# Kernel optimization log

Measured on AMD Instinct MI355X. Metric: run time of the kernel, lower is better.

Reference implementation:

```python
import jax, jax.numpy as jnp
import numpy as np
import math

D_MODEL = 1024
FEAT = 16            # feature_dim
HEADS = 16
HEAD_DIM = D_MODEL // HEADS          # 64
EXP = 1 + FEAT + FEAT * FEAT         # 273, expanded (Taylor) feature dim
BATCH = 4
SEQ = 2048


def taylor_exp(x):
    """2nd-order Taylor feature map: [1, x/d^{1/4}, (x ox x)/(sqrt(2)*sqrt(d))]."""
    d = x.shape[-1]
    r2 = math.sqrt(2.0)
    rd = math.sqrt(d)
    rrd = math.sqrt(rd)
    x2 = (x[..., :, None] * x[..., None, :]).reshape(*x.shape[:-1], d * d) / r2
    return jnp.concatenate([jnp.ones_like(x[..., :1]), x / rrd, x2 / rd], axis=-1)


def setup_inputs() -> dict:
    key = jax.random.key(0)
    ks = jax.random.split(key, 9)
    s_in = 1.0 / math.sqrt(D_MODEL)
    inp = {
        "x": jax.random.normal(ks[0], (BATCH, SEQ, D_MODEL), dtype=jnp.float32),
        "kv_state": jnp.zeros((BATCH, HEADS, EXP, HEAD_DIM), dtype=jnp.float32),
        "k_state": jnp.zeros((BATCH, HEADS, EXP), dtype=jnp.float32),
        # Linear params stored as [in, out] (y = x @ W + b)
        "Wq": jax.random.normal(ks[1], (D_MODEL, FEAT * HEADS), dtype=jnp.float32) * s_in,
        "bq": jnp.zeros((FEAT * HEADS,), dtype=jnp.float32),
        "Wk": jax.random.normal(ks[2], (D_MODEL, FEAT * HEADS), dtype=jnp.float32) * s_in,
        "bk": jnp.zeros((FEAT * HEADS,), dtype=jnp.float32),
        "Wv": jax.random.normal(ks[3], (D_MODEL, HEAD_DIM * HEADS), dtype=jnp.float32) * s_in,
        "bv": jnp.zeros((HEAD_DIM * HEADS,), dtype=jnp.float32),
        "Wo": jax.random.normal(ks[4], (HEADS * HEAD_DIM, D_MODEL), dtype=jnp.float32) * s_in,
        "bo": jnp.zeros((D_MODEL,), dtype=jnp.float32),
    }
    return inp


def _forward(x, kv_state, k_state, Wq, bq, Wk, bk, Wv, bv, Wo, bo):
    b, l, _ = x.shape
    # projections -> b h l d
    q = (x @ Wq + bq).reshape(b, l, HEADS, FEAT).transpose(0, 2, 1, 3)
    k = (x @ Wk + bk).reshape(b, l, HEADS, FEAT).transpose(0, 2, 1, 3)
    v = (x @ Wv + bv).reshape(b, l, HEADS, HEAD_DIM).transpose(0, 2, 1, 3)
    q = taylor_exp(q)  # b h l EXP
    k = taylor_exp(k)  # b h l EXP

    # scan over time: carry (kv_state [b,h,EXP,hd], k_state [b,h,EXP])
    qs = jnp.moveaxis(q, 2, 0)  # l b h EXP
    ks = jnp.moveaxis(k, 2, 0)  # l b h EXP
    vs = jnp.moveaxis(v, 2, 0)  # l b h hd

    def step(carry, qkv_t):
        kv, kst = carry
        q_t, k_t, v_t = qkv_t
        kv = kv + k_t[..., :, None] * v_t[..., None, :]   # b h EXP hd
        kst = kst + k_t                                    # b h EXP
        num = jnp.einsum('bhd,bhdc->bhc', q_t, kv)
        den = jnp.einsum('bhd,bhd->bh', q_t, kst) + 1e-6
        return (kv, kst), num / den[..., None]

    (kv_f, kst_f), outs = jax.lax.scan(step, (kv_state, k_state), (qs, ks, vs))
    # outs: l b h hd -> b l (h hd)
    y = jnp.moveaxis(outs, 0, 1).reshape(b, l, HEADS * HEAD_DIM)
    y = y @ Wo + bo  # dropout is identity in eval mode
    return y, kv_f, kst_f


def reference(x, kv_state, k_state, Wq, bq, Wk, bk, Wv, bv, Wo, bo):
    return _forward(x, kv_state, k_state, Wq, bq, Wk, bk, Wv, bv, Wo, bo)
```

## Files before the change

### kernel.cpp

```cpp
#include <hip/hip_runtime.h>

typedef unsigned short u16;
typedef __attribute__((ext_vector_type(8))) short bf16x8;
typedef __attribute__((ext_vector_type(4))) float f32x4;

#define BATCH 4
#define SEQ   2048
#define DM    1024
#define HEADS 16
#define FEAT  16
#define HD    64
#define EXPD  273
#define EXPP  288
#define CHK   128
#define NC    16
#define BH    64
#define QKS   512
#define MROWS 8192
#define C2    0.17677669529663687f

__device__ __forceinline__ u16 f2b(float f) {
  union { float f; unsigned u; } v; v.f = f;
  unsigned u = v.u;
  return (u16)((u + 0x7fffu + ((u >> 16) & 1u)) >> 16);
}
__device__ __forceinline__ float b2f(u16 s) {
  union { unsigned u; float f; } v; v.u = ((unsigned)s) << 16; return v.f;
}

typedef const unsigned int __attribute__((address_space(1)))* gas1;
typedef unsigned int __attribute__((address_space(3)))* las3;
__device__ __forceinline__ void gl_lds16(const u16* g, u16* l) {
  __builtin_amdgcn_global_load_lds((gas1)(const void*)g, (las3)(void*)l, 16, 0, 0);
}

__global__ __launch_bounds__(256) void prep(const float* __restrict__ x, u16* __restrict__ xb,
                                            const float* __restrict__ Wq, const float* __restrict__ Wk,
                                            const float* __restrict__ Wv, const float* __restrict__ Wo,
                                            u16* __restrict__ wqkvT, u16* __restrict__ woT,
                                            const float* __restrict__ bq, const float* __restrict__ bk,
                                            const float* __restrict__ bv, float* __restrict__ bias_all) {
  __shared__ float tile[32][33];
  int id = blockIdx.x;
  if (id < 8192) {
    int i = id * 256 + threadIdx.x;
    float4 v = ((const float4*)x)[i];
    u16 r[4] = {f2b(v.x), f2b(v.y), f2b(v.z), f2b(v.w)};
    ((uint2*)xb)[i] = *(uint2*)r;
    return;
  }
  id -= 8192;
  if (id < 2560) {
    const float* src; u16* dst; int N, t;
    if (id < 256)       { src = Wq; dst = wqkvT;            N = 256;  t = id; }
    else if (id < 512)  { src = Wk; dst = wqkvT + 256 * DM; N = 256;  t = id - 256; }
    else if (id < 1536) { src = Wv; dst = wqkvT + 512 * DM; N = 1024; t = id - 512; }
    else                { src = Wo; dst = woT;              N = 1024; t = id - 1536; }
    int nt = N / 32;
    int n0 = (t % nt) * 32, k0 = (t / nt) * 32;
    int tx = threadIdx.x & 31, ty = threadIdx.x >> 5;
    for (int i = ty; i < 32; i += 8)
      tile[i][tx] = src[(size_t)(k0 + i) * N + n0 + tx];
    __syncthreads();
    for (int i = ty; i < 32; i += 8)
      dst[(size_t)(n0 + i) * DM + k0 + tx] = f2b(tile[tx][i]);
    return;
  }
  id -= 2560;
  int i = id * 256 + threadIdx.x;
  float v;
  if (i < 256) v = bq[i];
  else if (i < 512) v = bk[i - 256];
  else v = bv[i - 512];
  bias_all[i] = v;
}

__global__ __launch_bounds__(256, 2) void gemmQKV(const u16* __restrict__ A, const u16* __restrict__ BT,
                                                  const float* __restrict__ bias,
                                                  float* __restrict__ qkw, u16* __restrict__ vbT) {
  __shared__ __align__(16) u16 As[2][128 * 32];
  __shared__ __align__(16) u16 Bs[2][256 * 32];
  const int tid = threadIdx.x;
  const int wave = tid >> 6, lane = tid & 63, qd = lane >> 4, ln = lane & 15;
  const int wr = (wave >> 1) * 64, wc = (wave & 1) * 128;
  const int m0 = blockIdx.y * 128, n0 = blockIdx.x * 256;
  const int K = DM;
  f32x4 acc[4][8];
#pragma unroll
  for (int i = 0; i < 4; i++)
#pragma unroll
    for (int j = 0; j < 8; j++) acc[i][j] = (f32x4){0.f, 0.f, 0.f, 0.f};
  const int sr = tid >> 2;
  const int scs = (((tid & 3) ^ ((sr >> 1) & 3))) * 8;
  const u16* gA0 = A + (size_t)(m0 + sr) * K + scs;
  const u16* gA1 = gA0 + (size_t)64 * K;
  const u16* gB0 = BT + (size_t)(n0 + sr) * K + scs;
  auto stage = [&](int buf, int kk) {
    gl_lds16(gA0 + kk, &As[buf][wave * 512]);
    gl_lds16(gA1 + kk, &As[buf][2048 + wave * 512]);
    gl_lds16(gB0 + kk,                    &Bs[buf][wave * 512]);
    gl_lds16(gB0 + (size_t)64 * K + kk,   &Bs[buf][2048 + wave * 512]);
    gl_lds16(gB0 + (size_t)128 * K + kk,  &Bs[buf][4096 + wave * 512]);
    gl_lds16(gB0 + (size_t)192 * K + kk,  &Bs[buf][6144 + wave * 512]);
  };
  const int swz = ((ln >> 1) & 3) << 3;
  auto compute = [&](int buf) {
    bf16x8 af[4], bf[8];
#pragma unroll
    for (int t = 0; t < 4; t++)
      af[t] = *(const bf16x8*)&As[buf][(wr + t * 16 + ln) * 32 + ((qd * 8) ^ swz)];
#pragma unroll
    for (int u = 0; u < 8; u++)
      bf[u] = *(const bf16x8*)&Bs[buf][(wc + u * 16 + ln) * 32 + ((qd * 8) ^ swz)];
#pragma unroll
    for (int mt = 0; mt < 4; mt++)
#pragma unroll
      for (int nt = 0; nt < 8; nt++)
        acc[mt][nt] = __builtin_amdgcn_mfma_f32_16x16x32_bf16(af[mt], bf[nt], acc[mt][nt], 0, 0, 0);
  };
  stage(0, 0);
  int buf = 0;
  for (int kk = 32; kk < K; kk += 32) {
    stage(buf ^ 1, kk);
    asm volatile("s_waitcnt vmcnt(6)" ::: "memory");
    __builtin_amdgcn_s_barrier();
    asm volatile("" ::: "memory");
    compute(buf);
    asm volatile("" ::: "memory");
    __builtin_amdgcn_s_barrier();
    buf ^= 1;
  }
  asm volatile("s_waitcnt vmcnt(0)" ::: "memory");
  __builtin_amdgcn_s_barrier();
  asm volatile("" ::: "memory");
  compute(buf);
  if (n0 < 512) {
#pragma unroll
    for (int nt = 0; nt < 8; nt++) {
      int col = n0 + wc + nt * 16 + ln;
      float bv = bias[col];
#pragma unroll
      for (int mt = 0; mt < 4; mt++)
#pragma unroll
        for (int r = 0; r < 4; r++) {
          int row = m0 + wr + mt * 16 + qd * 4 + r;
          qkw[(size_t)row * QKS + col] = acc[mt][nt][r] + bv;
        }
    }
  } else {
#pragma unroll
    for (int nt = 0; nt < 8; nt++) {
      int col = n0 + wc + nt * 16 + ln;
      float bv = bias[col];
      int vcol = col - 512;
#pragma unroll
      for (int mt = 0; mt < 4; mt++) {
        u16 pk[4];
#pragma unroll
        for (int r = 0; r < 4; r++) pk[r] = f2b(acc[mt][nt][r] + bv);
        int row0 = m0 + wr + mt * 16 + qd * 4;
        *(uint2*)&vbT[(size_t)vcol * MROWS + row0] = *(uint2*)pk;
      }
    }
  }
}

__global__ __launch_bounds__(256, 2) void gemm128(const u16* __restrict__ A, const u16* __restrict__ BT,
                                                  const float* __restrict__ bias, int M, int N, int K,
                                                  float* __restrict__ outF) {
  __shared__ __align__(16) u16 As[2][128 * 32];
  __shared__ __align__(16) u16 Bs[2][256 * 32];
  const int tid = threadIdx.x;
  const int wave = tid >> 6, lane = tid & 63, qd = lane >> 4, ln = lane & 15;
  const int wr = (wave >> 1) * 64, wc = (wave & 1) * 128;
  const int m0 = blockIdx.y * 128, n0 = blockIdx.x * 256;
  f32x4 acc[4][8];
#pragma unroll
  for (int i = 0; i < 4; i++)
#pragma unroll
    for (int j = 0; j < 8; j++) acc[i][j] = (f32x4){0.f, 0.f, 0.f, 0.f};
  const int sr = tid >> 2;
  const int scs = (((tid & 3) ^ ((sr >> 1) & 3))) * 8;
  const u16* gA0 = A + (size_t)(m0 + sr) * K + scs;
  const u16* gA1 = gA0 + (size_t)64 * K;
  const u16* gB0 = BT + (size_t)(n0 + sr) * K + scs;
  auto stage = [&](int buf, int kk) {
    gl_lds16(gA0 + kk, &As[buf][wave * 512]);
    gl_lds16(gA1 + kk, &As[buf][2048 + wave * 512]);
    gl_lds16(gB0 + kk,                    &Bs[buf][wave * 512]);
    gl_lds16(gB0 + (size_t)64 * K + kk,   &Bs[buf][2048 + wave * 512]);
    gl_lds16(gB0 + (size_t)128 * K + kk,  &Bs[buf][4096 + wave * 512]);
    gl_lds16(gB0 + (size_t)192 * K + kk,  &Bs[buf][6144 + wave * 512]);
  };
  const int swz = ((ln >> 1) & 3) << 3;
  auto compute = [&](int buf) {
    bf16x8 af[4], bf[8];
#pragma unroll
    for (int t = 0; t < 4; t++)
      af[t] = *(const bf16x8*)&As[buf][(wr + t * 16 + ln) * 32 + ((qd * 8) ^ swz)];
#pragma unroll
    for (int u = 0; u < 8; u++)
      bf[u] = *(const bf16x8*)&Bs[buf][(wc + u * 16 + ln) * 32 + ((qd * 8) ^ swz)];
#pragma unroll
    for (int mt = 0; mt < 4; mt++)
#pragma unroll
      for (int nt = 0; nt < 8; nt++)
        acc[mt][nt] = __builtin_amdgcn_mfma_f32_16x16x32_bf16(af[mt], bf[nt], acc[mt][nt], 0, 0, 0);
  };
  stage(0, 0);
  int buf = 0;
  for (int kk = 32; kk < K; kk += 32) {
    stage(buf ^ 1, kk);
    asm volatile("s_waitcnt vmcnt(6)" ::: "memory");
    __builtin_amdgcn_s_barrier();
    asm volatile("" ::: "memory");
    compute(buf);
    asm volatile("" ::: "memory");
    __builtin_amdgcn_s_barrier();
    buf ^= 1;
  }
  asm volatile("s_waitcnt vmcnt(0)" ::: "memory");
  __builtin_amdgcn_s_barrier();
  asm volatile("" ::: "memory");
  compute(buf);
#pragma unroll
  for (int nt = 0; nt < 8; nt++) {
    int col = n0 + wc + nt * 16 + ln;
    float bv = bias[col];
#pragma unroll
    for (int mt = 0; mt < 4; mt++)
#pragma unroll
      for (int r = 0; r < 4; r++) {
        int row = m0 + wr + mt * 16 + qd * 4 + r;
        outF[(size_t)row * N + col] = acc[mt][nt][r] + bv;
      }
  }
}

template<int KT>
__device__ __forceinline__ void feat_row(const float* q16, int p, u16* dst) {
  u16 pk[16];
  if (KT == 0 && p == 0) {
    pk[0] = 0x3F80;
#pragma unroll
    for (int j = 1; j < 16; j++) pk[j] = f2b(0.5f * q16[j - 1]);
  } else if (KT == 0) {
    pk[0] = f2b(0.5f * q16[15]);
    float wm = C2 * q16[0];
#pragma unroll
    for (int j = 1; j < 16; j++) pk[j] = f2b(wm * q16[j - 1]);
  } else {
    constexpr int c = 2 * KT;
    float wm = C2 * (p ? q16[c]     : q16[c - 1]);
    float w0 = C2 * (p ? q16[c - 1] : q16[c - 2]);
    pk[0] = f2b(w0 * q16[15]);
#pragma unroll
    for (int j = 1; j < 16; j++) pk[j] = f2b(wm * q16[j - 1]);
    if (KT == 8 && p) {
#pragma unroll
      for (int j = 1; j < 16; j++) pk[j] = 0;
    }
  }
  *(uint4*)dst = *(uint4*)pk;
  *(uint4*)(dst + 8) = *(uint4*)(pk + 8);
}

template<int MTB>
__device__ __forceinline__ void kfeat(const float* k16, int p, int t2, u16 (*kfT)[16][136]) {
  u16 pk[16];
  if (MTB == 0) {
    if (p == 0) {
      pk[0] = 0x3F80;
#pragma unroll
      for (int j = 1; j < 16; j++) pk[j] = f2b(0.5f * k16[j - 1]);
    } else {
      float w0 = C2 * k16[0], wm = C2 * k16[1];
      pk[0] = f2b(w0 * k16[15]);
#pragma unroll
      for (int j = 1; j < 16; j++) pk[j] = f2b(wm * k16[j - 1]);
    }
  } else if (MTB == 1) {
    if (p == 0) {
      pk[0] = f2b(0.5f * k16[15]);
      float wm = C2 * k16[0];
#pragma unroll
      for (int j = 1; j < 16; j++) pk[j] = f2b(wm * k16[j - 1]);
    } else {
      float w0 = C2 * k16[1], wm = C2 * k16[2];
      pk[0] = f2b(w0 * k16[15]);
#pragma unroll
      for (int j = 1; j < 16; j++) pk[j] = f2b(wm * k16[j - 1]);
    }
  } else {
    float wm = C2 * (p ? k16[MTB + 1] : k16[MTB - 1]);
    float w0 = C2 * (p ? k16[MTB]     : k16[MTB - 2]);
    pk[0] = f2b(w0 * k16[15]);
#pragma unroll
    for (int j = 1; j < 16; j++) pk[j] = f2b(wm * k16[j - 1]);
  }
  int b = 2 * p + (MTB & 1);
#pragma unroll
  for (int el = 0; el < 16; el++) kfT[b][el][t2] = pk[el];
}

__global__ __launch_bounds__(256) void chunk_sums(const float* __restrict__ qkw, const u16* __restrict__ vbT,
                                                  u16* __restrict__ ckvT, float* __restrict__ ck) {
  __shared__ float kl[CHK][20];
  __shared__ __align__(16) u16 kfT[4][16][136];
  const int tid = threadIdx.x;
  const int bh = blockIdx.x / NC, c = blockIdx.x % NC;
  const int b = bh >> 4, h = bh & 15;
  const int wave = tid >> 6, lane = tid & 63, qd = lane >> 4, ln = lane & 15;
  const int t2 = tid >> 1, p = tid & 1;
  const size_t rowbase = (size_t)(b * SEQ + c * CHK);
  float k16[16];
  {
    const float* kp = &qkw[(rowbase + t2) * QKS + 256 + h * FEAT];
    float4 v0 = *(const float4*)kp, v1 = *(const float4*)(kp + 4);
    float4 v2 = *(const float4*)(kp + 8), v3 = *(const float4*)(kp + 12);
    k16[0] = v0.x; k16[1] = v0.y; k16[2] = v0.z; k16[3] = v0.w;
    k16[4] = v1.x; k16[5] = v1.y; k16[6] = v1.z; k16[7] = v1.w;
    k16[8] = v2.x; k16[9] = v2.y; k16[10] = v2.z; k16[11] = v2.w;
    k16[12] = v3.x; k16[13] = v3.y; k16[14] = v3.z; k16[15] = v3.w;
    float4 h0, h1;
    if (p == 0) { h0 = v0; h1 = v1; } else { h0 = v2; h1 = v3; }
    *(float4*)&kl[t2][p * 8] = h0;
    *(float4*)&kl[t2][p * 8 + 4] = h1;
  }
  uint4 bVv[4][4];
#pragma unroll
  for (int kk2 = 0; kk2 < 4; kk2++)
#pragma unroll
    for (int nt = 0; nt < 4; nt++)
      bVv[kk2][nt] = *(const uint4*)&vbT[(size_t)(h * HD + nt * 16 + ln) * MROWS +
                                         rowbase + kk2 * 32 + qd * 8];
  const size_t obase = (size_t)(bh * NC + c) * HD;
  auto mstore = [&](int mt, int bufw) {
    f32x4 acc[4];
#pragma unroll
    for (int nt = 0; nt < 4; nt++) acc[nt] = (f32x4){0.f, 0.f, 0.f, 0.f};
#pragma unroll
    for (int kk2 = 0; kk2 < 4; kk2++) {
      bf16x8 a = *(const bf16x8*)&kfT[bufw][ln][kk2 * 32 + qd * 8];
#pragma unroll
      for (int nt = 0; nt < 4; nt++) {
        bf16x8 bb = *(const bf16x8*)&bVv[kk2][nt];
        acc[nt] = __builtin_amdgcn_mfma_f32_16x16x32_bf16(a, bb, acc[nt], 0, 0, 0);
      }
    }
#pragma unroll
    for (int nt = 0; nt < 4; nt++) {
      u16 pk[4];
#pragma unroll
      for (int r = 0; r < 4; r++) pk[r] = f2b(acc[nt][r]);
      *(uint2*)&ckvT[(obase + nt * 16 + ln) * EXPP + mt * 16 + qd * 4] = *(uint2*)pk;
    }
  };
  __syncthreads();
  kfeat<0>(k16, p, t2, kfT); kfeat<1>(k16, p, t2, kfT);
  __syncthreads();
  mstore(wave, wave);
  __syncthreads();
  kfeat<4>(k16, p, t2, kfT); kfeat<5>(k16, p, t2, kfT);
  __syncthreads();
  mstore(4 + wave, wave);
  __syncthreads();
  kfeat<8>(k16, p, t2, kfT); kfeat<9>(k16, p, t2, kfT);
  __syncthreads();
  mstore(8 + wave, wave);
  __syncthreads();
  kfeat<12>(k16, p, t2, kfT); kfeat<13>(k16, p, t2, kfT);
  __syncthreads();
  mstore(12 + wave, wave);
  __syncthreads();
  {
    u16 pk[16];
    if (p == 0) {
      float w0 = C2 * k16[14], wm = C2 * k16[15];
      pk[0] = f2b(w0 * k16[15]);
#pragma unroll
      for (int j = 1; j < 16; j++) pk[j] = f2b(wm * k16[j - 1]);
    } else {
      pk[0] = f2b(C2 * k16[15] * k16[15]);
#pragma unroll
      for (int j = 1; j < 16; j++) pk[j] = 0;
    }
#pragma unroll
    for (int el = 0; el < 16; el++) kfT[p][el][t2] = pk[el];
  }
  __syncthreads();
  if (wave < 2) mstore(16 + wave, wave);
  for (int e = tid; e < EXPP; e += 256) {
    float s = 0.f;
    if (e == 0) s = (float)CHK;
    else if (e < 17) { float t = 0.f; for (int tt = 0; tt < CHK; tt++) t += kl[tt][e - 1]; s = 0.5f * t; }
    else if (e < EXPD) {
      int u = e - 17, i0 = u >> 4, j0 = u & 15; float t = 0.f;
      for (int tt = 0; tt < CHK; tt++) t += kl[tt][i0] * kl[tt][j0];
      s = C2 * t;
    }
    ck[(size_t)(bh * NC + c) * EXPP + e] = s;
  }
}

__global__ __launch_bounds__(256) void kv_prefix(u16* __restrict__ ckvT, const float* __restrict__ kv0,
                                                 float* __restrict__ out_kv,
                                                 float* __restrict__ ck, const float* __restrict__ k0,
                                                 float* __restrict__ out_k) {
  const int tid = threadIdx.x;
  const int bh = blockIdx.x / 10, eg = blockIdx.x % 10;
  if (eg == 9) {
    for (int e = tid; e < EXPP; e += 256) {
      float S = (e < EXPD) ? k0[(size_t)bh * EXPD + e] : 0.f;
      for (int c = 0; c < NC; c++) {
        size_t idx = ((size_t)bh * NC + c) * EXPP + e;
        float v = ck[idx];
        ck[idx] = S;
        S += v;
      }
      if (e < EXPD) out_k[(size_t)bh * EXPD + e] = S;
    }
    return;
  }
  const int hd = tid >> 2;
  const int e0 = eg * 32 + (tid & 3) * 8;
  float S[8];
#pragma unroll
  for (int j = 0; j < 8; j++) {
    int e = e0 + j;
    S[j] = (e < EXPD) ? kv0[((size_t)bh * EXPD + e) * HD + hd] : 0.f;
  }
  u16* base = ckvT + ((size_t)bh * NC * HD + hd) * EXPP + e0;
  const size_t cstride = (size_t)HD * EXPP;
  uint4 v0 = *(const uint4*)base;
  uint4 v1 = *(const uint4*)(base + cstride);
  for (int c = 0; c < NC; c++) {
    uint4 vn = v1;
    if (c + 2 < NC) vn = *(const uint4*)(base + (size_t)(c + 2) * cstride);
    union { uint4 q; u16 s[8]; } pk;
#pragma unroll
    for (int j = 0; j < 8; j++) pk.s[j] = f2b(S[j]);
    *(uint4*)(base + (size_t)c * cstride) = pk.q;
    union { uint4 q; u16 s[8]; } vv; vv.q = v0;
#pragma unroll
    for (int j = 0; j < 8; j++) S[j] += b2f(vv.s[j]);
    v0 = v1; v1 = vn;
  }
#pragma unroll
  for (int j = 0; j < 8; j++) {
    int e = e0 + j;
    if (e < EXPD) out_kv[((size_t)bh * EXPD + e) * HD + hd] = S[j];
  }
}

__global__ __launch_bounds__(256) void out_chunk(const float* __restrict__ qkw, const u16* __restrict__ vbT,
                                                 const u16* __restrict__ ckvT, const float* __restrict__ ck,
                                                 u16* __restrict__ ob) {
  __shared__ __align__(16) u16 pool[18432];
  __shared__ float kstl[EXPP];
  __shared__ float denl[CHK];
  u16 (*qlb)[40] = (u16(*)[40])pool;
  u16 (*klb)[32] = (u16(*)[32])(pool + 5120);
  u16 (*qfs)[40] = (u16(*)[40])(pool + 9216);
  u16 (*alB)[72] = (u16(*)[72])pool;
  u16 (*alA)[72] = (u16(*)[72])(pool + 9216);
  const int tid = threadIdx.x;
  const int bh = blockIdx.x / NC, c = blockIdx.x % NC;
  const int b = bh >> 4, h = bh & 15;
  const int wave = tid >> 6, lane = tid & 63, qd = lane >> 4, ln = lane & 15;
  const int t2 = tid >> 1, p = tid & 1;
  const size_t rowbase = (size_t)(b * SEQ + c * CHK);
  float q16[16];
  {
    const float* qp = &qkw[(rowbase + t2) * QKS + h * FEAT];
    float4 v0 = *(const float4*)qp, v1 = *(const float4*)(qp + 4);
    float4 v2 = *(const float4*)(qp + 8), v3 = *(const float4*)(qp + 12);
    q16[0] = v0.x; q16[1] = v0.y; q16[2] = v0.z; q16[3] = v0.w;
    q16[4] = v1.x; q16[5] = v1.y; q16[6] = v1.z; q16[7] = v1.w;
    q16[8] = v2.x; q16[9] = v2.y; q16[10] = v2.z; q16[11] = v2.w;
    q16[12] = v3.x; q16[13] = v3.y; q16[14] = v3.z; q16[15] = v3.w;
    u16 qb[8];
#pragma unroll
    for (int j = 0; j < 8; j++) qb[j] = f2b(q16[p * 8 + j]);
    *(uint4*)&qlb[t2][p * 8] = *(uint4*)qb;
    *(uint4*)&qlb[t2][16 + p * 8] = (uint4){0u, 0u, 0u, 0u};
    const float* kp = &qkw[(rowbase + t2) * QKS + 256 + h * FEAT + p * 8];
    float4 k0v = *(const float4*)kp, k1v = *(const float4*)(kp + 4);
    u16 kb[8] = {f2b(k0v.x), f2b(k0v.y), f2b(k0v.z), f2b(k0v.w),
                 f2b(k1v.x), f2b(k1v.y), f2b(k1v.z), f2b(k1v.w)};
    *(uint4*)&klb[t2][p * 8] = *(uint4*)kb;
    *(uint4*)&klb[t2][16 + p * 8] = (uint4){0u, 0u, 0u, 0u};
  }
  const size_t cbase = (size_t)(bh * NC + c);
  for (int e = tid; e < EXPP; e += 256) kstl[e] = ck[cbase * EXPP + e];
  const u16* sptr = ckvT + (cbase * HD + wave * 16 + ln) * EXPP + qd * 8;
  uint4 bSv[9];
#pragma unroll
  for (int kt = 0; kt < 9; kt++) bSv[kt] = *(const uint4*)(sptr + kt * 32);
  uint4 bVv[4];
#pragma unroll
  for (int kk2 = 0; kk2 < 4; kk2++)
    bVv[kk2] = *(const uint4*)&vbT[(size_t)(h * HD + wave * 16 + ln) * MROWS +
                                   rowbase + kk2 * 32 + qd * 8];
  feat_row<0>(q16, p, &qfs[t2][p * 16]);
  __syncthreads();
  f32x4 accO[8];
#pragma unroll
  for (int nt = 0; nt < 8; nt++) accO[nt] = (f32x4){0.f, 0.f, 0.f, 0.f};
#define KSTEP(KT)                                                                          \
  {                                                                                        \
    bf16x8 aS = *(const bf16x8*)&bSv[(KT)];                                                \
    _Pragma("unroll")                                                                      \
    for (int nt = 0; nt < 8; nt++) {                                                       \
      bf16x8 bQ = *(const bf16x8*)&qfs[nt * 16 + ln][qd * 8];                              \
      accO[nt] = __builtin_amdgcn_mfma_f32_16x16x32_bf16(aS, bQ, accO[nt], 0, 0, 0);       \
    }                                                                                      \
    __syncthreads();                                                                       \
    if ((KT) < 8) {                                                                        \
      feat_row<(KT) + 1>(q16, p, &qfs[t2][p * 16]);                                        \
      __syncthreads();                                                                     \
    }                                                                                      \
  }
  KSTEP(0) KSTEP(1) KSTEP(2) KSTEP(3) KSTEP(4) KSTEP(5) KSTEP(6) KSTEP(7) KSTEP(8)
#undef KSTEP
  {
    f32x4 accU[8];
    bf16x8 aK = *(const bf16x8*)&klb[wave * 16 + ln][qd * 8];
#pragma unroll
    for (int nt = 0; nt < 8; nt++) {
      bf16x8 bQ = *(const bf16x8*)&qlb[nt * 16 + ln][qd * 8];
      accU[nt] = __builtin_amdgcn_mfma_f32_16x16x32_bf16(aK, bQ, (f32x4){0.f, 0.f, 0.f, 0.f}, 0, 0, 0);
    }
#pragma unroll
    for (int nt = 0; nt < 8; nt++) {
      int t = nt * 16 + ln, sb = wave * 16 + qd * 4;
      u16 pk[4];
#pragma unroll
      for (int r = 0; r < 4; r++) {
        float u = accU[nt][r];
        float sc = 1.f + 0.25f * u + 0.03125f * u * u;
        pk[r] = (sb + r <= t) ? f2b(sc) : (u16)0;
      }
      *(uint2*)&alA[t][sb] = *(uint2*)pk;
    }
  }
  {
    f32x4 accU[8];
    bf16x8 aK = *(const bf16x8*)&klb[(wave + 4) * 16 + ln][qd * 8];
#pragma unroll
    for (int nt = 0; nt < 8; nt++) {
      bf16x8 bQ = *(const bf16x8*)&qlb[nt * 16 + ln][qd * 8];
      accU[nt] = __builtin_amdgcn_mfma_f32_16x16x32_bf16(aK, bQ, (f32x4){0.f, 0.f, 0.f, 0.f}, 0, 0, 0);
    }
    __syncthreads();
#pragma unroll
    for (int nt = 0; nt < 8; nt++) {
      int t = nt * 16 + ln, sbl = wave * 16 + qd * 4;
      u16 pk[4];
#pragma unroll
      for (int r = 0; r < 4; r++) {
        float u = accU[nt][r];
        float sc = 1.f + 0.25f * u + 0.03125f * u * u;
        pk[r] = (64 + sbl + r <= t) ? f2b(sc) : (u16)0;
      }
      *(uint2*)&alB[t][sbl] = *(uint2*)pk;
    }
  }
  __syncthreads();
#pragma unroll
  for (int kk2 = 0; kk2 < 4; kk2++) {
    bf16x8 aV = *(const bf16x8*)&bVv[kk2];
#pragma unroll
    for (int nt = 0; nt < 8; nt++) {
      bf16x8 bA = (kk2 < 2) ? *(const bf16x8*)&alA[nt * 16 + ln][kk2 * 32 + qd * 8]
                            : *(const bf16x8*)&alB[nt * 16 + ln][(kk2 - 2) * 32 + qd * 8];
      accO[nt] = __builtin_amdgcn_mfma_f32_16x16x32_bf16(aV, bA, accO[nt], 0, 0, 0);
    }
  }
  {
    float s = 0.f;
#pragma unroll
    for (int i2 = 0; i2 < 8; i2++) {
      int i = p * 8 + i2;
      float inner = 0.f;
#pragma unroll
      for (int j = 0; j < 16; j++) inner += q16[j] * kstl[17 + i * 16 + j];
      s += q16[i] * inner;
    }
    s *= C2;
    float s1 = 0.f;
#pragma unroll
    for (int j2 = 0; j2 < 8; j2++) s1 += q16[p * 8 + j2] * kstl[1 + p * 8 + j2];
    s += 0.5f * s1;
    if (p == 0) s += kstl[0] + 1e-6f;
    const u16* arow = p ? &alB[t2][0] : &alA[t2][0];
    float da = 0.f;
#pragma unroll
    for (int sb = 0; sb < 8; sb++) {
      union { uint4 q; u16 hh[8]; } uu;
      uu.q = *(const uint4*)(arow + sb * 8);
#pragma unroll
      for (int j = 0; j < 8; j++) da += b2f(uu.hh[j]);
    }
    s += da;
    s += __shfl_xor(s, 1);
    if (p == 0) denl[t2] = s;
  }
  __syncthreads();
#pragma unroll
  for (int nt = 0; nt < 8; nt++) {
    int t = nt * 16 + ln;
    float dn = denl[t];
    u16 pk[4];
#pragma unroll
    for (int r = 0; r < 4; r++) pk[r] = f2b(accO[nt][r] / dn);
    *(uint2*)&ob[(rowbase + t) * DM + h * HD + wave * 16 + qd * 4] = *(uint2*)pk;
  }
}

extern "C" void kernel_launch(void* const* d_in, const int* in_sizes, int n_in,
                              void* d_out, int out_size, void* d_ws, size_t ws_size,
                              hipStream_t stream) {
  (void)in_sizes; (void)n_in; (void)out_size;
  const float* x   = (const float*)d_in[0];
  const float* kv0 = (const float*)d_in[1];
  const float* k0  = (const float*)d_in[2];
  const float* bq  = (const float*)d_in[4];
  const float* bk  = (const float*)d_in[6];
  const float* bv  = (const float*)d_in[8];
  const float* bo  = (const float*)d_in[10];
  float* out = (float*)d_out;
  char* ws = (char*)d_ws;
  size_t off = 0;
  auto take = [&](size_t bytes) { char* p = ws + off; off += (bytes + 255) & ~(size_t)255; return p; };
  u16*   xb     = (u16*)  take((size_t)BATCH * SEQ * DM * 2);
  u16*   wqkvT  = (u16*)  take((size_t)1536 * DM * 2);
  u16*   woT    = (u16*)  take((size_t)DM * DM * 2);
  float* bias_a = (float*)take((size_t)1536 * 4);
  float* qkw    = (float*)take((size_t)BATCH * SEQ * QKS * 4);
  u16*   vbT    = (u16*)  take((size_t)BATCH * SEQ * DM * 2);
  u16*   ckvT   = (u16*)  take((size_t)BH * NC * EXPP * HD * 2);
  float* ck     = (float*)take((size_t)BH * NC * EXPP * 4);
  u16*   ob     = (u16*)  take((size_t)BATCH * SEQ * DM * 2);
  if (off > ws_size) return;

  float* out_kv = out + (size_t)BATCH * SEQ * DM;
  float* out_k  = out_kv + (size_t)BH * EXPD * HD;

  prep<<<8192 + 2560 + 6, 256, 0, stream>>>(x, xb,
      (const float*)d_in[3], (const float*)d_in[5], (const float*)d_in[7], (const float*)d_in[9],
      wqkvT, woT, bq, bk, bv, bias_a);

  gemmQKV<<<dim3(6, 64), 256, 0, stream>>>(xb, wqkvT, bias_a, qkw, vbT);

  chunk_sums<<<BH * NC, 256, 0, stream>>>(qkw, vbT, ckvT, ck);
  kv_prefix<<<BH * 10, 256, 0, stream>>>(ckvT, kv0, out_kv, ck, k0, out_k);
  out_chunk<<<BH * NC, 256, 0, stream>>>(qkw, vbT, ckvT, ck, ob);

  gemm128<<<dim3(4, 64), 256, 0, stream>>>(ob, woT, bo, MROWS, DM, DM, out);
}
```

Measured before the change: 294.0 us.

## Shrink GEMM tiles for more blocks and double-buffer out_chunk feature staging

The QKV GEMM moves from 256-wide to 192-wide N tiles, giving 8x64 blocks, and the output GEMM moves to 128x128 tiles with 3-block occupancy, giving 512 blocks. The aim is better CU fill on the chip. In out_chunk, the Taylor feature tiles are now double-buffered so the next feature row is built while MFMAs consume the current one, which cuts one barrier per step. The denominator polynomial is also hoisted earlier. Smaller tiles reduce data reuse per block, and the extra LDS buffer raises out_chunk shared-memory use.

```diff
diff --git a/kernel.cpp b/kernel.cpp
--- a/kernel.cpp
+++ b/kernel.cpp
@@ -79,17 +79,17 @@
                                                   const float* __restrict__ bias,
                                                   float* __restrict__ qkw, u16* __restrict__ vbT) {
   __shared__ __align__(16) u16 As[2][128 * 32];
-  __shared__ __align__(16) u16 Bs[2][256 * 32];
+  __shared__ __align__(16) u16 Bs[2][192 * 32];
   const int tid = threadIdx.x;
   const int wave = tid >> 6, lane = tid & 63, qd = lane >> 4, ln = lane & 15;
-  const int wr = (wave >> 1) * 64, wc = (wave & 1) * 128;
-  const int m0 = blockIdx.y * 128, n0 = blockIdx.x * 256;
+  const int wr = (wave >> 1) * 64, wc = (wave & 1) * 96;
+  const int m0 = blockIdx.y * 128, n0 = blockIdx.x * 192;
   const int K = DM;
-  f32x4 acc[4][8];
+  f32x4 acc[4][6];
 #pragma unroll
   for (int i = 0; i < 4; i++)
 #pragma unroll
-    for (int j = 0; j < 8; j++) acc[i][j] = (f32x4){0.f, 0.f, 0.f, 0.f};
+    for (int j = 0; j < 6; j++) acc[i][j] = (f32x4){0.f, 0.f, 0.f, 0.f};
   const int sr = tid >> 2;
   const int scs = (((tid & 3) ^ ((sr >> 1) & 3))) * 8;
   const u16* gA0 = A + (size_t)(m0 + sr) * K + scs;
@@ -98,31 +98,30 @@
   auto stage = [&](int buf, int kk) {
     gl_lds16(gA0 + kk, &As[buf][wave * 512]);
     gl_lds16(gA1 + kk, &As[buf][2048 + wave * 512]);
-    gl_lds16(gB0 + kk,                    &Bs[buf][wave * 512]);
-    gl_lds16(gB0 + (size_t)64 * K + kk,   &Bs[buf][2048 + wave * 512]);
-    gl_lds16(gB0 + (size_t)128 * K + kk,  &Bs[buf][4096 + wave * 512]);
-    gl_lds16(gB0 + (size_t)192 * K + kk,  &Bs[buf][6144 + wave * 512]);
+    gl_lds16(gB0 + kk,                   &Bs[buf][wave * 512]);
+    gl_lds16(gB0 + (size_t)64 * K + kk,  &Bs[buf][2048 + wave * 512]);
+    gl_lds16(gB0 + (size_t)128 * K + kk, &Bs[buf][4096 + wave * 512]);
   };
   const int swz = ((ln >> 1) & 3) << 3;
   auto compute = [&](int buf) {
-    bf16x8 af[4], bf[8];
+    bf16x8 af[4], bf[6];
 #pragma unroll
     for (int t = 0; t < 4; t++)
       af[t] = *(const bf16x8*)&As[buf][(wr + t * 16 + ln) * 32 + ((qd * 8) ^ swz)];
 #pragma unroll
-    for (int u = 0; u < 8; u++)
+    for (int u = 0; u < 6; u++)
       bf[u] = *(const bf16x8*)&Bs[buf][(wc + u * 16 + ln) * 32 + ((qd * 8) ^ swz)];
 #pragma unroll
     for (int mt = 0; mt < 4; mt++)
 #pragma unroll
-      for (int nt = 0; nt < 8; nt++)
+      for (int nt = 0; nt < 6; nt++)
         acc[mt][nt] = __builtin_amdgcn_mfma_f32_16x16x32_bf16(af[mt], bf[nt], acc[mt][nt], 0, 0, 0);
   };
   stage(0, 0);
   int buf = 0;
   for (int kk = 32; kk < K; kk += 32) {
     stage(buf ^ 1, kk);
-    asm volatile("s_waitcnt vmcnt(6)" ::: "memory");
+    asm volatile("s_waitcnt vmcnt(5)" ::: "memory");
     __builtin_amdgcn_s_barrier();
     asm volatile("" ::: "memory");
     compute(buf);
@@ -134,11 +133,11 @@
   __builtin_amdgcn_s_barrier();
   asm volatile("" ::: "memory");
   compute(buf);
-  if (n0 < 512) {
-#pragma unroll
-    for (int nt = 0; nt < 8; nt++) {
-      int col = n0 + wc + nt * 16 + ln;
-      float bv = bias[col];
+#pragma unroll
+  for (int nt = 0; nt < 6; nt++) {
+    int col = n0 + wc + nt * 16 + ln;
+    float bv = bias[col];
+    if (col < 512) {
 #pragma unroll
       for (int mt = 0; mt < 4; mt++)
 #pragma unroll
@@ -146,12 +145,7 @@
           int row = m0 + wr + mt * 16 + qd * 4 + r;
           qkw[(size_t)row * QKS + col] = acc[mt][nt][r] + bv;
         }
-    }
-  } else {
-#pragma unroll
-    for (int nt = 0; nt < 8; nt++) {
-      int col = n0 + wc + nt * 16 + ln;
-      float bv = bias[col];
+    } else {
       int vcol = col - 512;
 #pragma unroll
       for (int mt = 0; mt < 4; mt++) {
@@ -165,53 +159,52 @@
   }
 }
 
-__global__ __launch_bounds__(256, 2) void gemm128(const u16* __restrict__ A, const u16* __restrict__ BT,
+__global__ __launch_bounds__(256, 3) void gemm128(const u16* __restrict__ A, const u16* __restrict__ BT,
                                                   const float* __restrict__ bias, int M, int N, int K,
                                                   float* __restrict__ outF) {
   __shared__ __align__(16) u16 As[2][128 * 32];
-  __shared__ __align__(16) u16 Bs[2][256 * 32];
+  __shared__ __align__(16) u16 Bs[2][128 * 32];
   const int tid = threadIdx.x;
   const int wave = tid >> 6, lane = tid & 63, qd = lane >> 4, ln = lane & 15;
-  const int wr = (wave >> 1) * 64, wc = (wave & 1) * 128;
-  const int m0 = blockIdx.y * 128, n0 = blockIdx.x * 256;
-  f32x4 acc[4][8];
+  const int wr = (wave >> 1) * 64, wc = (wave & 1) * 64;
+  const int m0 = blockIdx.y * 128, n0 = blockIdx.x * 128;
+  f32x4 acc[4][4];
 #pragma unroll
   for (int i = 0; i < 4; i++)
 #pragma unroll
-    for (int j = 0; j < 8; j++) acc[i][j] = (f32x4){0.f, 0.f, 0.f, 0.f};
+    for (int j = 0; j < 4; j++) acc[i][j] = (f32x4){0.f, 0.f, 0.f, 0.f};
   const int sr = tid >> 2;
   const int scs = (((tid & 3) ^ ((sr >> 1) & 3))) * 8;
   const u16* gA0 = A + (size_t)(m0 + sr) * K + scs;
   const u16* gA1 = gA0 + (size_t)64 * K;
   const u16* gB0 = BT + (size_t)(n0 + sr) * K + scs;
+  const u16* gB1 = gB0 + (size_t)64 * K;
   auto stage = [&](int buf, int kk) {
     gl_lds16(gA0 + kk, &As[buf][wave * 512]);
     gl_lds16(gA1 + kk, &As[buf][2048 + wave * 512]);
-    gl_lds16(gB0 + kk,                    &Bs[buf][wave * 512]);
-    gl_lds16(gB0 + (size_t)64 * K + kk,   &Bs[buf][2048 + wave * 512]);
-    gl_lds16(gB0 + (size_t)128 * K + kk,  &Bs[buf][4096 + wave * 512]);
-    gl_lds16(gB0 + (size_t)192 * K + kk,  &Bs[buf][6144 + wave * 512]);
+    gl_lds16(gB0 + kk, &Bs[buf][wave * 512]);
+    gl_lds16(gB1 + kk, &Bs[buf][2048 + wave * 512]);
   };
   const int swz = ((ln >> 1) & 3) << 3;
   auto compute = [&](int buf) {
-    bf16x8 af[4], bf[8];
+    bf16x8 af[4], bf[4];
 #pragma unroll
     for (int t = 0; t < 4; t++)
       af[t] = *(const bf16x8*)&As[buf][(wr + t * 16 + ln) * 32 + ((qd * 8) ^ swz)];
 #pragma unroll
-    for (int u = 0; u < 8; u++)
+    for (int u = 0; u < 4; u++)
       bf[u] = *(const bf16x8*)&Bs[buf][(wc + u * 16 + ln) * 32 + ((qd * 8) ^ swz)];
 #pragma unroll
     for (int mt = 0; mt < 4; mt++)
 #pragma unroll
-      for (int nt = 0; nt < 8; nt++)
+      for (int nt = 0; nt < 4; nt++)
         acc[mt][nt] = __builtin_amdgcn_mfma_f32_16x16x32_bf16(af[mt], bf[nt], acc[mt][nt], 0, 0, 0);
   };
   stage(0, 0);
   int buf = 0;
   for (int kk = 32; kk < K; kk += 32) {
     stage(buf ^ 1, kk);
-    asm volatile("s_waitcnt vmcnt(6)" ::: "memory");
+    asm volatile("s_waitcnt vmcnt(4)" ::: "memory");
     __builtin_amdgcn_s_barrier();
     asm volatile("" ::: "memory");
     compute(buf);
@@ -224,7 +217,7 @@
   asm volatile("" ::: "memory");
   compute(buf);
 #pragma unroll
-  for (int nt = 0; nt < 8; nt++) {
+  for (int nt = 0; nt < 4; nt++) {
     int col = n0 + wc + nt * 16 + ln;
     float bv = bias[col];
 #pragma unroll
@@ -456,14 +449,15 @@
 __global__ __launch_bounds__(256) void out_chunk(const float* __restrict__ qkw, const u16* __restrict__ vbT,
                                                  const u16* __restrict__ ckvT, const float* __restrict__ ck,
                                                  u16* __restrict__ ob) {
-  __shared__ __align__(16) u16 pool[18432];
+  __shared__ __align__(16) u16 pool[19456];
   __shared__ float kstl[EXPP];
   __shared__ float denl[CHK];
-  u16 (*qlb)[40] = (u16(*)[40])pool;
-  u16 (*klb)[32] = (u16(*)[32])(pool + 5120);
-  u16 (*qfs)[40] = (u16(*)[40])(pool + 9216);
-  u16 (*alB)[72] = (u16(*)[72])pool;
-  u16 (*alA)[72] = (u16(*)[72])(pool + 9216);
+  u16 (*qlb)[40]  = (u16(*)[40])pool;
+  u16 (*klb)[32]  = (u16(*)[32])(pool + 5120);
+  u16 (*qfs0)[40] = (u16(*)[40])(pool + 9216);
+  u16 (*qfs1)[40] = (u16(*)[40])(pool + 14336);
+  u16 (*alB)[72]  = (u16(*)[72])pool;
+  u16 (*alA)[72]  = (u16(*)[72])(pool + 9216);
   const int tid = threadIdx.x;
   const int bh = blockIdx.x / NC, c = blockIdx.x % NC;
   const int b = bh >> 4, h = bh & 15;
@@ -502,27 +496,54 @@
   for (int kk2 = 0; kk2 < 4; kk2++)
     bVv[kk2] = *(const uint4*)&vbT[(size_t)(h * HD + wave * 16 + ln) * MROWS +
                                    rowbase + kk2 * 32 + qd * 8];
-  feat_row<0>(q16, p, &qfs[t2][p * 16]);
-  __syncthreads();
+  feat_row<0>(q16, p, &qfs0[t2][p * 16]);
   f32x4 accO[8];
 #pragma unroll
   for (int nt = 0; nt < 8; nt++) accO[nt] = (f32x4){0.f, 0.f, 0.f, 0.f};
-#define KSTEP(KT)                                                                          \
+#define KSTEP(KT, CUR, NXT)                                                                \
   {                                                                                        \
+    __syncthreads();                                                                       \
+    bf16x8 bQ[8];                                                                          \
+    _Pragma("unroll")                                                                      \
+    for (int nt = 0; nt < 8; nt++) bQ[nt] = *(const bf16x8*)&CUR[nt * 16 + ln][qd * 8];    \
+    feat_row<(KT) + 1>(q16, p, &NXT[t2][p * 16]);                                          \
     bf16x8 aS = *(const bf16x8*)&bSv[(KT)];                                                \
     _Pragma("unroll")                                                                      \
-    for (int nt = 0; nt < 8; nt++) {                                                       \
-      bf16x8 bQ = *(const bf16x8*)&qfs[nt * 16 + ln][qd * 8];                              \
-      accO[nt] = __builtin_amdgcn_mfma_f32_16x16x32_bf16(aS, bQ, accO[nt], 0, 0, 0);       \
-    }                                                                                      \
-    __syncthreads();                                                                       \
-    if ((KT) < 8) {                                                                        \
-      feat_row<(KT) + 1>(q16, p, &qfs[t2][p * 16]);                                        \
-      __syncthreads();                                                                     \
-    }                                                                                      \
-  }
-  KSTEP(0) KSTEP(1) KSTEP(2) KSTEP(3) KSTEP(4) KSTEP(5) KSTEP(6) KSTEP(7) KSTEP(8)
+    for (int nt = 0; nt < 8; nt++)                                                         \
+      accO[nt] = __builtin_amdgcn_mfma_f32_16x16x32_bf16(aS, bQ[nt], accO[nt], 0, 0, 0);   \
+  }
+  KSTEP(0, qfs0, qfs1) KSTEP(1, qfs1, qfs0) KSTEP(2, qfs0, qfs1) KSTEP(3, qfs1, qfs0)
+  KSTEP(4, qfs0, qfs1) KSTEP(5, qfs1, qfs0) KSTEP(6, qfs0, qfs1) KSTEP(7, qfs1, qfs0)
 #undef KSTEP
+  {
+    __syncthreads();
+    bf16x8 aS = *(const bf16x8*)&bSv[8];
+#pragma unroll
+    for (int nt = 0; nt < 8; nt++) {
+      bf16x8 bQ = *(const bf16x8*)&qfs0[nt * 16 + ln][qd * 8];
+      accO[nt] = __builtin_amdgcn_mfma_f32_16x16x32_bf16(aS, bQ, accO[nt], 0, 0, 0);
+    }
+  }
+  __syncthreads();
+  float s_poly;
+  {
+    float s = 0.f;
+#pragma unroll
+    for (int i2 = 0; i2 < 8; i2++) {
+      int i = p * 8 + i2;
+      float inner = 0.f;
+#pragma unroll
+      for (int j = 0; j < 16; j++) inner += q16[j] * kstl[17 + i * 16 + j];
+      s += q16[i] * inner;
+    }
+    s *= C2;
+    float s1 = 0.f;
+#pragma unroll
+    for (int j2 = 0; j2 < 8; j2++) s1 += q16[p * 8 + j2] * kstl[1 + p * 8 + j2];
+    s += 0.5f * s1;
+    if (p == 0) s += kstl[0] + 1e-6f;
+    s_poly = s;
+  }
   {
     f32x4 accU[8];
     bf16x8 aK = *(const bf16x8*)&klb[wave * 16 + ln][qd * 8];
@@ -578,21 +599,6 @@
     }
   }
   {
-    float s = 0.f;
-#pragma unroll
-    for (int i2 = 0; i2 < 8; i2++) {
-      int i = p * 8 + i2;
-      float inner = 0.f;
-#pragma unroll
-      for (int j = 0; j < 16; j++) inner += q16[j] * kstl[17 + i * 16 + j];
-      s += q16[i] * inner;
-    }
-    s *= C2;
-    float s1 = 0.f;
-#pragma unroll
-    for (int j2 = 0; j2 < 8; j2++) s1 += q16[p * 8 + j2] * kstl[1 + p * 8 + j2];
-    s += 0.5f * s1;
-    if (p == 0) s += kstl[0] + 1e-6f;
     const u16* arow = p ? &alB[t2][0] : &alA[t2][0];
     float da = 0.f;
 #pragma unroll
@@ -602,7 +608,7 @@
 #pragma unroll
       for (int j = 0; j < 8; j++) da += b2f(uu.hh[j]);
     }
-    s += da;
+    float s = s_poly + da;
     s += __shfl_xor(s, 1);
     if (p == 0) denl[t2] = s;
   }
@@ -651,11 +657,11 @@
       (const float*)d_in[3], (const float*)d_in[5], (const float*)d_in[7], (const float*)d_in[9],
       wqkvT, woT, bq, bk, bv, bias_a);
 
-  gemmQKV<<<dim3(6, 64), 256, 0, stream>>>(xb, wqkvT, bias_a, qkw, vbT);
+  gemmQKV<<<dim3(8, 64), 256, 0, stream>>>(xb, wqkvT, bias_a, qkw, vbT);
 
   chunk_sums<<<BH * NC, 256, 0, stream>>>(qkw, vbT, ckvT, ck);
   kv_prefix<<<BH * 10, 256, 0, stream>>>(ckvT, kv0, out_kv, ck, k0, out_k);
   out_chunk<<<BH * NC, 256, 0, stream>>>(qkw, vbT, ckvT, ck, ob);
 
-  gemm128<<<dim3(4, 64), 256, 0, stream>>>(ob, woT, bo, MROWS, DM, DM, out);
-}
+  gemm128<<<dim3(8, 64), 256, 0, stream>>>(ob, woT, bo, MROWS, DM, DM, out);
+}
```

New measurement: 284.8 us. 1.03x faster.
